# Kernel optimization log

Measured on AMD Instinct MI355X. Metric: run time of the kernel, lower is better.

## Reference

```python
import jax, jax.numpy as jnp
import numpy as np

T = 0.07  # temperature from __init__ default


def setup_inputs() -> dict:
    key = jax.random.key(0)
    ks = jax.random.split(key, 5)
    B, D, H, E = 4096, 2048, 2048, 128
    init = lambda k, shp, fan: jax.random.normal(k, shp, dtype=jnp.float32) * (1.0 / np.sqrt(fan))
    return {
        "input1": jax.random.normal(ks[0], (B, D), dtype=jnp.float32),
        "input2": jax.random.normal(ks[1], (B, D), dtype=jnp.float32),
        "W0": init(ks[2], (D, H), D), "b0": jnp.zeros((H,), jnp.float32),
        "W1": init(ks[3], (H, H), H), "b1": jnp.zeros((H,), jnp.float32),
        "W2": init(ks[4], (H, E), H), "b2": jnp.zeros((E,), jnp.float32),
    }


def _mlp(x, W0, b0, W1, b1, W2, b2):
    # Linear -> ReLU -> Linear -> Linear (ReLU only between hidden layers)
    x = jax.nn.relu(x @ W0 + b0)
    x = x @ W1 + b1
    return x @ W2 + b2


def reference(input1, input2, W0, b0, W1, b1, W2, b2):
    B = input1.shape[0]
    e1 = _mlp(input1, W0, b0, W1, b1, W2, b2)
    e2 = _mlp(input2, W0, b0, W1, b1, W2, b2)
    feats = jnp.stack([e1, e2], axis=1)                       # [B, 2, E]
    feats = feats / jnp.linalg.norm(feats, axis=2, keepdims=True)
    # view(N,2,dim).permute(1,0,2).reshape(2N,dim): view0 rows then view1 rows
    f = jnp.concatenate([feats[:, 0], feats[:, 1]], axis=0)   # [2B, E]
    N2 = 2 * B
    sim = (f @ f.T) / T                                        # [2B, 2B]
    idx = jnp.arange(N2)
    pos = sim[idx, (idx + B) % N2]                             # partner view similarity
    # exclude self-similarity (diagonal) from the logsumexp denominator
    sim = jnp.where(jnp.eye(N2, dtype=bool), jnp.float32(-1e9), sim)
    # CE with positive at index 0 of [pos, negatives] == -pos + logsumexp(non-self)
    loss = jnp.mean(jax.nn.logsumexp(sim, axis=1) - pos)
    return loss
```

## Files before the change

### kernel.cpp

```cpp
#include <hip/hip_runtime.h>
#include <stdint.h>

typedef float f32x4 __attribute__((ext_vector_type(4)));
typedef float f32x16 __attribute__((ext_vector_type(16)));
typedef __bf16 bf16x8 __attribute__((ext_vector_type(8)));
typedef unsigned short u16;
typedef unsigned int u32;

#define INVT 14.285714285714286f
#define L2E  1.4426950408889634f

__device__ __forceinline__ u16 f2bf(float f) {
  u32 u = __float_as_uint(f);
  u32 r = (u + 0x7fffu + ((u >> 16) & 1u)) >> 16;
  return (u16)r;
}
__device__ __forceinline__ float bf2f(u16 h) { return __uint_as_float(((u32)h) << 16); }

__device__ __forceinline__ void g2l16(const void* g, void* l) {
  auto gp = reinterpret_cast<__attribute__((address_space(1))) uint32_t*>(
      reinterpret_cast<uintptr_t>(g));
  auto lp = reinterpret_cast<__attribute__((address_space(3))) uint32_t*>(
      reinterpret_cast<uintptr_t>(l));
  __builtin_amdgcn_global_load_lds(gp, lp, 16, 0, 0);
}

__global__ __launch_bounds__(256) void k_prep(const float* __restrict__ in1,
                                              const float* __restrict__ in2,
                                              u16* __restrict__ Xb,
                                              const float* __restrict__ w0, u16* __restrict__ w0t,
                                              const float* __restrict__ w1, u16* __restrict__ w1t,
                                              const float* __restrict__ w2, u16* __restrict__ w2t) {
  const int bid = blockIdx.x;
  if (bid < 16384) {
    int i = (bid * 256 + threadIdx.x) * 4;
    float4 v;
    if (i < 8388608) v = *(const float4*)(in1 + i);
    else             v = *(const float4*)(in2 + (i - 8388608));
    ushort4 p;
    p.x = f2bf(v.x); p.y = f2bf(v.y); p.z = f2bf(v.z); p.w = f2bf(v.w);
    *(ushort4*)(Xb + i) = p;
    return;
  }
  __shared__ float t[64][65];
  const float* in; u16* out; int R, C, r0, c0;
  if (bid < 18432) {
    const int f = bid - 16384;
    const int z = f >> 10, rem = f & 1023;
    in = z ? w1 : w0; out = z ? w1t : w0t; R = 2048; C = 2048;
    r0 = (rem >> 5) * 64; c0 = (rem & 31) * 64;
  } else {
    const int f = bid - 18432;
    in = w2; out = w2t; R = 2048; C = 128;
    r0 = (f >> 1) * 64; c0 = (f & 1) * 64;
  }
#pragma unroll
  for (int p = 0; p < 16; ++p) {
    int idx = p * 256 + threadIdx.x;
    int r = idx >> 6, c = idx & 63;
    t[r][c] = in[(size_t)(r0 + r) * C + (c0 + c)];
  }
  __syncthreads();
#pragma unroll
  for (int p = 0; p < 16; ++p) {
    int idx = p * 256 + threadIdx.x;
    int c = idx >> 6, r = idx & 63;
    out[(size_t)(c0 + c) * R + (r0 + r)] = f2bf(t[r][c]);
  }
}

__global__ __launch_bounds__(512, 2) void k_gemm(const u16* __restrict__ A, const u16* __restrict__ Bt,
                                                 const float* __restrict__ bias, u16* __restrict__ C,
                                                 int M, int N, int K, int relu) {
  __shared__ __align__(16) u16 sm[65536];
  const int tid = threadIdx.x;
  const int l = tid & 63, w = tid >> 6;
  const int wm = w >> 2, wn = w & 3;
  const int lm = l & 31, c0 = l >> 5;
  const int m0 = blockIdx.y * 256, n0 = blockIdx.x * 256;

  const char* gA = (const char*)(A + (size_t)(m0 + w * 32 + lm) * K + c0 * 8);
  const char* gB = (const char*)(Bt + (size_t)(n0 + w * 32 + lm) * K + c0 * 8);

  auto issue_half = [&](int t, int part, int stg) {
    const int h = part >> 1, isB = part & 1;
    const char* g = (isB ? gB : gA) + (size_t)t * 128 + h * 64;
    char* lb = (char*)sm + stg * 65536 + isB * 32768 + h * 16384 + w * 1024 + l * 16;
    g2l16(g, lb);
    g2l16(g + 32, lb + 8192);
  };

  f32x16 acc[4][2] = {};
  const int NT = K >> 6;

  issue_half(0, 0, 0); issue_half(0, 1, 0); issue_half(0, 2, 0); issue_half(0, 3, 0);
  asm volatile("s_waitcnt vmcnt(4)" ::: "memory");
  asm volatile("s_barrier" ::: "memory");

  for (int kt = 0; kt < NT; ++kt) {
    const u16* bcur = sm + (kt & 1) * 32768;
    const int nstg = (kt & 1) ^ 1;
    const bool pf = (kt + 1) < NT;

#pragma unroll
    for (int k = 0; k < 4; ++k) {
      const u16* As = bcur + (k >> 1) * 8192;
      const u16* Bs = bcur + 16384 + (k >> 1) * 8192;
      const int fb = (k & 1) * 4096 + c0 * 256 + lm * 8;
      bf16x8 a4[4], b2[2];
#pragma unroll
      for (int fm = 0; fm < 4; ++fm)
        a4[fm] = *(const bf16x8*)(As + fb + (wm * 4 + fm) * 512);
#pragma unroll
      for (int fn = 0; fn < 2; ++fn)
        b2[fn] = *(const bf16x8*)(Bs + fb + (wn * 2 + fn) * 512);
      if (pf) issue_half(kt + 1, k, nstg);
      asm volatile("s_barrier" ::: "memory");
      asm volatile("s_waitcnt lgkmcnt(0)" ::: "memory");
      __builtin_amdgcn_s_setprio(1);
#pragma unroll
      for (int fm = 0; fm < 4; ++fm)
#pragma unroll
        for (int fn = 0; fn < 2; ++fn)
          acc[fm][fn] = __builtin_amdgcn_mfma_f32_32x32x16_bf16(a4[fm], b2[fn],
                                                                acc[fm][fn], 0, 0, 0);
      __builtin_amdgcn_s_setprio(0);
      if (k & 1) {
        if (pf) asm volatile("s_waitcnt vmcnt(4)" ::: "memory");
        else    asm volatile("s_waitcnt vmcnt(0)" ::: "memory");
      }
      asm volatile("s_barrier" ::: "memory");
    }
  }

  const int colb = n0 + wn * 64 + lm;
  const int rowb = m0 + wm * 128 + 4 * c0;
#pragma unroll
  for (int fn = 0; fn < 2; ++fn) {
    const float b = bias[colb + fn * 32];
#pragma unroll
    for (int fm = 0; fm < 4; ++fm)
#pragma unroll
      for (int g = 0; g < 4; ++g)
#pragma unroll
        for (int rr = 0; rr < 4; ++rr) {
          float v = acc[fm][fn][g * 4 + rr] + b;
          if (relu) v = fmaxf(v, 0.0f);
          C[(size_t)(rowb + fm * 32 + g * 8 + rr) * N + colb + fn * 32] = f2bf(v);
        }
  }
}

__global__ __launch_bounds__(256, 2) void k_gemm_sk(const u16* __restrict__ A, const u16* __restrict__ Bt,
                                                    float* __restrict__ Ep, int K, int Ksplit) {
  __shared__ __align__(16) u16 sm[24576];
  const int tid = threadIdx.x;
  const int l = tid & 63, w = tid >> 6;
  const int wm = w >> 1, wn = w & 1;
  const int m0 = blockIdx.y * 128;
  const int split = blockIdx.x;
  const int k0s = split * Ksplit;

  const int kb = ((l & 3) ^ ((l >> 3) & 3)) * 16;
  const char* gA = (const char*)(A + (size_t)(m0 + w * 16 + (l >> 2)) * K + k0s) + kb;
  const char* gB = (const char*)(Bt + (size_t)(w * 16 + (l >> 2)) * K + k0s) + kb;
  const size_t radv = (size_t)64 * K * 2;

  auto issue = [&](int kcB, int stg) {
    char* base = (char*)sm + stg * 16384;
    char* dA = base + w * 1024 + l * 16;
    char* dB = base + 8192 + w * 1024 + l * 16;
    g2l16(gA + kcB, dA);
    g2l16(gA + radv + kcB, dA + 4096);
    g2l16(gB + kcB, dB);
    g2l16(gB + radv + kcB, dB + 4096);
  };

  const int lm = l & 31;
  const int c0 = l >> 5;
  const int sw = (lm >> 1) & 3;

  f32x16 acc[2][2] = {};

  auto compute = [&](int stg) {
    const u16* As = sm + stg * 8192;
    const u16* Bs = As + 4096;
#pragma unroll
    for (int t = 0; t < 2; ++t) {
      const int cc = (((t << 1) + c0) ^ sw) * 8;
      bf16x8 a2[2], b2[2];
#pragma unroll
      for (int fm = 0; fm < 2; ++fm) a2[fm] = *(const bf16x8*)(As + (wm * 64 + fm * 32 + lm) * 32 + cc);
#pragma unroll
      for (int fn = 0; fn < 2; ++fn) b2[fn] = *(const bf16x8*)(Bs + (wn * 64 + fn * 32 + lm) * 32 + cc);
#pragma unroll
      for (int fm = 0; fm < 2; ++fm)
#pragma unroll
        for (int fn = 0; fn < 2; ++fn)
          acc[fm][fn] = __builtin_amdgcn_mfma_f32_32x32x16_bf16(a2[fm], b2[fn],
                                                                acc[fm][fn], 0, 0, 0);
    }
  };

  const int NK = Ksplit >> 5;
  issue(0, 0);
  issue(64, 1);
  int st = 0;
  for (int kt = 0; kt < NK; ++kt) {
    if (kt + 1 < NK) asm volatile("s_waitcnt vmcnt(4)" ::: "memory");
    else             asm volatile("s_waitcnt vmcnt(0)" ::: "memory");
    asm volatile("s_barrier" ::: "memory");
    if (kt + 2 < NK) {
      int stp = st + 2; if (stp >= 3) stp -= 3;
      issue((kt + 2) * 64, stp);
    }
    compute(st);
    ++st; if (st == 3) st = 0;
  }

  const int colb = wn * 64 + lm;
  const int rowb = m0 + wm * 64 + 4 * c0;
#pragma unroll
  for (int fn = 0; fn < 2; ++fn)
#pragma unroll
    for (int fm = 0; fm < 2; ++fm)
#pragma unroll
      for (int g = 0; g < 4; ++g)
#pragma unroll
        for (int rr = 0; rr < 4; ++rr)
          Ep[((size_t)split * 8192 + rowb + fm * 32 + g * 8 + rr) * 128 + colb + fn * 32] =
              acc[fm][fn][g * 4 + rr];
}

__global__ __launch_bounds__(256) void k_norm(const float* __restrict__ Ep,
                                              const float* __restrict__ b2, u16* __restrict__ F) {
  const int l = threadIdx.x & 63, w = threadIdx.x >> 6;
  const int row = blockIdx.x * 4 + w;
  const float2* base = (const float2*)Ep + (size_t)row * 64 + l;
  float x = 0.f, y = 0.f;
#pragma unroll
  for (int s = 0; s < 4; ++s) {
    float2 t = base[(size_t)s * (8192 * 64)];
    x += t.x; y += t.y;
  }
  x += b2[l * 2]; y += b2[l * 2 + 1];
  float sq = x * x + y * y;
#pragma unroll
  for (int off = 1; off < 64; off <<= 1) sq += __shfl_xor(sq, off);
  const float inv = 1.0f / sqrtf(sq);
  F[(size_t)row * 128 + l * 2] = f2bf(x * inv);
  F[(size_t)row * 128 + l * 2 + 1] = f2bf(y * inv);
}

__global__ __launch_bounds__(256, 2) void k_sim(const u16* __restrict__ F, float* __restrict__ Sp) {
  __shared__ __align__(16) u16 sm[32768];
  const int tid = threadIdx.x;
  const int l = tid & 63, w = tid >> 6;
  const int wm = w >> 1, wn = w & 1;
  const int lm = l & 31, c0 = l >> 5;
  const int r0 = blockIdx.y * 128;
  const int cb0 = blockIdx.x * 1024;

  u16* B0 = sm;
  u16* AB1 = sm + 16384;

  const int srow0 = tid >> 4;
  const int schunk = tid & 15;
  auto stage = [&](const u16* src, u16* dst) {
#pragma unroll
    for (int j = 0; j < 8; ++j) {
      const int row = j * 16 + srow0;
      const int lc = schunk ^ (row & 7);
      g2l16((const char*)(src + (size_t)row * 128) + lc * 16,
            (char*)dst + j * 4096 + tid * 16);
    }
  };

  stage(F + (size_t)r0 * 128, AB1);
  asm volatile("s_waitcnt vmcnt(0)" ::: "memory");
  __syncthreads();

  bf16x8 a[2][8];
#pragma unroll
  for (int fm = 0; fm < 2; ++fm) {
    const int ra = wm * 64 + fm * 32 + lm;
#pragma unroll
    for (int kf = 0; kf < 8; ++kf)
      a[fm][kf] = *(const bf16x8*)(AB1 + ra * 128 + (((kf << 1) + c0) ^ (ra & 7)) * 8);
  }
  asm volatile("s_waitcnt lgkmcnt(0)" ::: "memory");

  stage(F + (size_t)cb0 * 128, B0);

  const float S2 = INVT * L2E;
  const int rB = wn * 64 + lm;
  f32x16 runS[2] = {};

#pragma unroll 1
  for (int p = 0; p < 8; ++p) {
    asm volatile("s_waitcnt vmcnt(0)" ::: "memory");
    asm volatile("s_barrier" ::: "memory");
    if (p < 7) stage(F + (size_t)(cb0 + (p + 1) * 128) * 128, (p & 1) ? B0 : AB1);
    const u16* Bs = (p & 1) ? AB1 : B0;

    f32x16 acc[2][2] = {};
#pragma unroll
    for (int kf = 0; kf < 8; ++kf) {
      const int kc = (kf << 1) + c0;
      bf16x8 b0v = *(const bf16x8*)(Bs + rB * 128 + (kc ^ (rB & 7)) * 8);
      bf16x8 b1v = *(const bf16x8*)(Bs + (rB + 32) * 128 + (kc ^ ((rB + 32) & 7)) * 8);
      acc[0][0] = __builtin_amdgcn_mfma_f32_32x32x16_bf16(a[0][kf], b0v, acc[0][0], 0, 0, 0);
      acc[0][1] = __builtin_amdgcn_mfma_f32_32x32x16_bf16(a[0][kf], b1v, acc[0][1], 0, 0, 0);
      acc[1][0] = __builtin_amdgcn_mfma_f32_32x32x16_bf16(a[1][kf], b0v, acc[1][0], 0, 0, 0);
      acc[1][1] = __builtin_amdgcn_mfma_f32_32x32x16_bf16(a[1][kf], b1v, acc[1][1], 0, 0, 0);
    }

    const int cp = cb0 + p * 128;
    if (cp == r0) {
#pragma unroll
      for (int fm = 0; fm < 2; ++fm)
#pragma unroll
        for (int fn = 0; fn < 2; ++fn) {
          const int rcol = wn * 64 + fn * 32 + lm;
#pragma unroll
          for (int r = 0; r < 16; ++r) {
            const int rrow = wm * 64 + fm * 32 + (r & 3) + 8 * (r >> 2) + 4 * c0;
            float e = exp2f(fmaf(acc[fm][fn][r], S2, -S2));
            if (rrow == rcol) e = 0.f;
            runS[fm][r] += e;
          }
        }
    } else {
#pragma unroll
      for (int fm = 0; fm < 2; ++fm)
#pragma unroll
        for (int fn = 0; fn < 2; ++fn)
#pragma unroll
          for (int r = 0; r < 16; ++r)
            runS[fm][r] += exp2f(fmaf(acc[fm][fn][r], S2, -S2));
    }
  }

#pragma unroll
  for (int fm = 0; fm < 2; ++fm)
#pragma unroll
    for (int r = 0; r < 16; ++r) {
      float s = runS[fm][r];
      s += __shfl_xor(s, 1);
      s += __shfl_xor(s, 2);
      s += __shfl_xor(s, 4);
      s += __shfl_xor(s, 8);
      s += __shfl_xor(s, 16);
      runS[fm][r] = s;
    }

  __syncthreads();
  float* red = (float*)sm;
  if (wn == 0) {
    if (lm == 0) {
#pragma unroll
      for (int fm = 0; fm < 2; ++fm)
#pragma unroll
        for (int r = 0; r < 16; ++r)
          red[wm * 64 + fm * 32 + (r & 3) + 8 * (r >> 2) + 4 * c0] = runS[fm][r];
    }
  }
  __syncthreads();
  if (wn == 1 && lm == 0) {
#pragma unroll
    for (int fm = 0; fm < 2; ++fm)
#pragma unroll
      for (int r = 0; r < 16; ++r) {
        const int rr = wm * 64 + fm * 32 + (r & 3) + 8 * (r >> 2) + 4 * c0;
        Sp[(size_t)blockIdx.x * 8192 + r0 + rr] = red[rr] + runS[fm][r];
      }
  }
}

__global__ __launch_bounds__(256) void k_combine(const float* __restrict__ Sp,
                                                 const u16* __restrict__ F,
                                                 float* __restrict__ out) {
  const int r = blockIdx.x * 256 + threadIdx.x;
  float S = 0.f;
#pragma unroll
  for (int c = 0; c < 8; ++c) S += Sp[c * 8192 + r];
  const float lse = INVT + logf(S);
  const int par = (r + 4096) & 8191;
  const bf16x8* a = (const bf16x8*)(F + (size_t)r * 128);
  const bf16x8* b = (const bf16x8*)(F + (size_t)par * 128);
  float dot = 0.f;
#pragma unroll
  for (int k = 0; k < 16; ++k) {
    bf16x8 va = a[k], vb = b[k];
#pragma unroll
    for (int j = 0; j < 8; ++j) dot = fmaf((float)va[j], (float)vb[j], dot);
  }
  float contrib = lse - dot * INVT;
#pragma unroll
  for (int off = 1; off < 64; off <<= 1) contrib += __shfl_xor(contrib, off);
  if ((threadIdx.x & 63) == 0) atomicAdd(out, contrib * (1.0f / 8192.0f));
}

extern "C" void kernel_launch(void* const* d_in, const int* in_sizes, int n_in,
                              void* d_out, int out_size, void* d_ws, size_t ws_size,
                              hipStream_t stream) {
  const float* input1 = (const float*)d_in[0];
  const float* input2 = (const float*)d_in[1];
  const float* W0 = (const float*)d_in[2];
  const float* b0 = (const float*)d_in[3];
  const float* W1 = (const float*)d_in[4];
  const float* b1 = (const float*)d_in[5];
  const float* W2 = (const float*)d_in[6];
  const float* b2 = (const float*)d_in[7];
  float* out = (float*)d_out;
  char* ws = (char*)d_ws;

  u16* Xb = (u16*)(ws + 0);
  u16* H1 = (u16*)(ws + 33554432);
  u16* W0T = (u16*)(ws + 67108864);
  u16* W1T = (u16*)(ws + 75497472);
  float* Ep = (float*)(ws + 67108864);
  u16* W2T = (u16*)(ws + 83886080);
  float* Sp = (float*)(ws + 83886080);
  u16* Ff = (u16*)(ws + 84410368);
  u16* H2 = Xb;

  hipMemsetAsync(d_out, 0, sizeof(float), stream);
  k_prep<<<18496, 256, 0, stream>>>(input1, input2, Xb, W0, W0T, W1, W1T, W2, W2T);
  k_gemm<<<dim3(8, 32), 512, 0, stream>>>(Xb, W0T, b0, H1, 8192, 2048, 2048, 1);
  k_gemm<<<dim3(8, 32), 512, 0, stream>>>(H1, W1T, b1, H2, 8192, 2048, 2048, 0);
  k_gemm_sk<<<dim3(4, 64), 256, 0, stream>>>(H2, W2T, Ep, 2048, 512);
  k_norm<<<2048, 256, 0, stream>>>(Ep, b2, Ff);
  k_sim<<<dim3(8, 64), 256, 0, stream>>>(Ff, Sp);
  k_combine<<<32, 256, 0, stream>>>(Sp, Ff, out);
}
```

Baseline: 350.0 us.

## Store GEMM operands in k-slab blocked layout for contiguous LDS loads

The prep kernel now writes the bf16 inputs and the transposed W0/W1 in a blocked layout: 16-element k-slabs, each holding 32-row groups of 512 contiguous elements. The GEMM loader now fetches a whole 1KB contiguous chunk per wave per slab instead of row-strided 64-byte pieces. The first GEMM writes its output H1 in the same blocked layout so the second GEMM can consume it directly. The aim is fully coalesced global-to-LDS loads and a cheaper weight transpose without shared memory, at the cost of scattered 2-byte stores in the first GEMM's epilogue.

Result: faster. 339.6 us (-3.0%).

```diff
diff --git a/kernel.cpp b/kernel.cpp
--- a/kernel.cpp
+++ b/kernel.cpp
@@ -24,6 +24,7 @@
       reinterpret_cast<uintptr_t>(l));
   __builtin_amdgcn_global_load_lds(gp, lp, 16, 0, 0);
 }
+
 
 __global__ __launch_bounds__(256) void k_prep(const float* __restrict__ in1,
                                               const float* __restrict__ in2,
@@ -32,46 +33,73 @@
                                               const float* __restrict__ w1, u16* __restrict__ w1t,
                                               const float* __restrict__ w2, u16* __restrict__ w2t) {
   const int bid = blockIdx.x;
-  if (bid < 16384) {
-    int i = (bid * 256 + threadIdx.x) * 4;
-    float4 v;
-    if (i < 8388608) v = *(const float4*)(in1 + i);
-    else             v = *(const float4*)(in2 + (i - 8388608));
-    ushort4 p;
-    p.x = f2bf(v.x); p.y = f2bf(v.y); p.z = f2bf(v.z); p.w = f2bf(v.w);
-    *(ushort4*)(Xb + i) = p;
+  const int tid = threadIdx.x;
+  if (bid < 8192) {
+    const int l = tid & 63, w = tid >> 6;
+    const int lm = l & 31, ch = l >> 5;
+    const int u = bid * 4 + w;
+    const int s = u & 127, g = u >> 7;
+    const float* src = (g < 128 ? in1 : in2) +
+                       (size_t)((g & 127) * 32 + lm) * 2048 + s * 16 + ch * 8;
+    float4 v0 = *(const float4*)src;
+    float4 v1 = *(const float4*)(src + 4);
+    uint4 o;
+    o.x = (u32)f2bf(v0.x) | ((u32)f2bf(v0.y) << 16);
+    o.y = (u32)f2bf(v0.z) | ((u32)f2bf(v0.w) << 16);
+    o.z = (u32)f2bf(v1.x) | ((u32)f2bf(v1.y) << 16);
+    o.w = (u32)f2bf(v1.z) | ((u32)f2bf(v1.w) << 16);
+    *(uint4*)(Xb + (size_t)s * 131072 + g * 512 + l * 8) = o;
     return;
   }
+  if (bid < 12288) {
+    const int l = tid & 63, w = tid >> 6;
+    const int lm = l & 31, ch = l >> 5;
+    const int v = (bid - 8192) * 4 + w;
+    const int z = v >> 13, u2 = v & 8191;
+    const int s = u2 & 127, g = u2 >> 7;
+    const float* Wm = z ? w1 : w0;
+    u16* O = z ? w1t : w0t;
+    const float* src = Wm + (size_t)(s * 16 + ch * 8) * 2048 + g * 32 + lm;
+    float f0 = src[0];
+    float f1 = src[2048];
+    float f2 = src[2 * 2048];
+    float f3 = src[3 * 2048];
+    float f4 = src[4 * 2048];
+    float f5 = src[5 * 2048];
+    float f6 = src[6 * 2048];
+    float f7 = src[7 * 2048];
+    uint4 o;
+    o.x = (u32)f2bf(f0) | ((u32)f2bf(f1) << 16);
+    o.y = (u32)f2bf(f2) | ((u32)f2bf(f3) << 16);
+    o.z = (u32)f2bf(f4) | ((u32)f2bf(f5) << 16);
+    o.w = (u32)f2bf(f6) | ((u32)f2bf(f7) << 16);
+    *(uint4*)(O + (size_t)s * 32768 + g * 512 + l * 8) = o;
+    return;
+  }
   __shared__ float t[64][65];
-  const float* in; u16* out; int R, C, r0, c0;
-  if (bid < 18432) {
-    const int f = bid - 16384;
-    const int z = f >> 10, rem = f & 1023;
-    in = z ? w1 : w0; out = z ? w1t : w0t; R = 2048; C = 2048;
-    r0 = (rem >> 5) * 64; c0 = (rem & 31) * 64;
-  } else {
-    const int f = bid - 18432;
-    in = w2; out = w2t; R = 2048; C = 128;
-    r0 = (f >> 1) * 64; c0 = (f & 1) * 64;
-  }
+  const int f = bid - 12288;
+  const float* in = w2;
+  u16* out = w2t;
+  const int C = 128, R = 2048;
+  const int r0 = (f >> 1) * 64, c0t = (f & 1) * 64;
 #pragma unroll
   for (int p = 0; p < 16; ++p) {
-    int idx = p * 256 + threadIdx.x;
+    int idx = p * 256 + tid;
     int r = idx >> 6, c = idx & 63;
-    t[r][c] = in[(size_t)(r0 + r) * C + (c0 + c)];
+    t[r][c] = in[(size_t)(r0 + r) * C + (c0t + c)];
   }
   __syncthreads();
 #pragma unroll
   for (int p = 0; p < 16; ++p) {
-    int idx = p * 256 + threadIdx.x;
+    int idx = p * 256 + tid;
     int c = idx >> 6, r = idx & 63;
-    out[(size_t)(c0 + c) * R + (r0 + r)] = f2bf(t[r][c]);
+    out[(size_t)(c0t + c) * R + (r0 + r)] = f2bf(t[r][c]);
   }
 }
 
 __global__ __launch_bounds__(512, 2) void k_gemm(const u16* __restrict__ A, const u16* __restrict__ Bt,
                                                  const float* __restrict__ bias, u16* __restrict__ C,
-                                                 int M, int N, int K, int relu) {
+                                                 int M, int N, int K, int relu, int blockedC) {
   __shared__ __align__(16) u16 sm[65536];
   const int tid = threadIdx.x;
   const int l = tid & 63, w = tid >> 6;
@@ -79,15 +107,18 @@
   const int lm = l & 31, c0 = l >> 5;
   const int m0 = blockIdx.y * 256, n0 = blockIdx.x * 256;
 
-  const char* gA = (const char*)(A + (size_t)(m0 + w * 32 + lm) * K + c0 * 8);
-  const char* gB = (const char*)(Bt + (size_t)(n0 + w * 32 + lm) * K + c0 * 8);
+  const char* gA = (const char*)A + (size_t)((m0 >> 5) + w) * 1024 + l * 16;
+  const char* gB = (const char*)Bt + (size_t)((n0 >> 5) + w) * 1024 + l * 16;
+  const size_t slabA = (size_t)M * 32, slabB = (size_t)N * 32;
 
   auto issue_half = [&](int t, int part, int stg) {
     const int h = part >> 1, isB = part & 1;
-    const char* g = (isB ? gB : gA) + (size_t)t * 128 + h * 64;
+    const char* g = isB ? gB : gA;
+    const size_t slab = isB ? slabB : slabA;
+    const int s0 = t * 4 + h * 2;
     char* lb = (char*)sm + stg * 65536 + isB * 32768 + h * 16384 + w * 1024 + l * 16;
-    g2l16(g, lb);
-    g2l16(g + 32, lb + 8192);
+    g2l16(g + (size_t)s0 * slab, lb);
+    g2l16(g + (size_t)(s0 + 1) * slab, lb + 8192);
   };
 
   f32x16 acc[4][2] = {};
@@ -133,21 +164,43 @@
     }
   }
 
-  const int colb = n0 + wn * 64 + lm;
-  const int rowb = m0 + wm * 128 + 4 * c0;
-#pragma unroll
-  for (int fn = 0; fn < 2; ++fn) {
-    const float b = bias[colb + fn * 32];
-#pragma unroll
-    for (int fm = 0; fm < 4; ++fm)
-#pragma unroll
-      for (int g = 0; g < 4; ++g)
-#pragma unroll
-        for (int rr = 0; rr < 4; ++rr) {
-          float v = acc[fm][fn][g * 4 + rr] + b;
-          if (relu) v = fmaxf(v, 0.0f);
-          C[(size_t)(rowb + fm * 32 + g * 8 + rr) * N + colb + fn * 32] = f2bf(v);
-        }
+  if (blockedC) {
+#pragma unroll
+    for (int fn = 0; fn < 2; ++fn) {
+      const int col = n0 + wn * 64 + lm + fn * 32;
+      const float b = bias[col];
+      const int sc = col >> 4, cb = (col >> 3) & 1, e = col & 7;
+#pragma unroll
+      for (int fm = 0; fm < 4; ++fm) {
+        const int gg = (m0 >> 5) + wm * 4 + fm;
+        u16* base = C + (size_t)sc * ((size_t)M * 16) + gg * 512 + cb * 256 + e;
+#pragma unroll
+        for (int g = 0; g < 4; ++g)
+#pragma unroll
+          for (int rr = 0; rr < 4; ++rr) {
+            float v = acc[fm][fn][g * 4 + rr] + b;
+            if (relu) v = fmaxf(v, 0.0f);
+            base[(4 * c0 + g * 8 + rr) * 8] = f2bf(v);
+          }
+      }
+    }
+  } else {
+    const int colb = n0 + wn * 64 + lm;
+    const int rowb = m0 + wm * 128 + 4 * c0;
+#pragma unroll
+    for (int fn = 0; fn < 2; ++fn) {
+      const float b = bias[colb + fn * 32];
+#pragma unroll
+      for (int fm = 0; fm < 4; ++fm)
+#pragma unroll
+        for (int g = 0; g < 4; ++g)
+#pragma unroll
+          for (int rr = 0; rr < 4; ++rr) {
+            float v = acc[fm][fn][g * 4 + rr] + b;
+            if (relu) v = fmaxf(v, 0.0f);
+            C[(size_t)(rowb + fm * 32 + g * 8 + rr) * N + colb + fn * 32] = f2bf(v);
+          }
+    }
   }
 }
 
@@ -426,9 +479,9 @@
   u16* H2 = Xb;
 
   hipMemsetAsync(d_out, 0, sizeof(float), stream);
-  k_prep<<<18496, 256, 0, stream>>>(input1, input2, Xb, W0, W0T, W1, W1T, W2, W2T);
-  k_gemm<<<dim3(8, 32), 512, 0, stream>>>(Xb, W0T, b0, H1, 8192, 2048, 2048, 1);
-  k_gemm<<<dim3(8, 32), 512, 0, stream>>>(H1, W1T, b1, H2, 8192, 2048, 2048, 0);
+  k_prep<<<12352, 256, 0, stream>>>(input1, input2, Xb, W0, W0T, W1, W1T, W2, W2T);
+  k_gemm<<<dim3(8, 32), 512, 0, stream>>>(Xb, W0T, b0, H1, 8192, 2048, 2048, 1, 1);
+  k_gemm<<<dim3(8, 32), 512, 0, stream>>>(H1, W1T, b1, H2, 8192, 2048, 2048, 0, 0);
   k_gemm_sk<<<dim3(4, 64), 256, 0, stream>>>(H2, W2T, Ep, 2048, 512);
   k_norm<<<2048, 256, 0, stream>>>(Ep, b2, Ff);
   k_sim<<<dim3(8, 64), 256, 0, stream>>>(Ff, Sp);
```
